# Performance work log

Measured on AMD Instinct MI355X. Metric: run time of the kernel, lower is better.

Reference implementation:

```python
import jax, jax.numpy as jnp
import numpy as np

B, S, L = 256, 512, 128


def setup_inputs() -> dict:
    key = jax.random.key(0)
    k0, k1, k2, k3, k4, k5 = jax.random.split(key, 6)
    features = jax.random.normal(k0, (B, S, L), dtype=jnp.float32)
    attention_mask = jnp.ones((B, S), dtype=jnp.int32)  # all positions valid
    labels = jax.random.randint(k1, (B, S), 0, L)
    confidence = jax.random.uniform(k2, (B,), dtype=jnp.float32)
    start_transitions = jax.random.uniform(k3, (L,), minval=-0.1, maxval=0.1)
    end_transitions = jax.random.uniform(k4, (L,), minval=-0.1, maxval=0.1)
    transitions = jax.random.uniform(k5, (L, L), minval=-0.1, maxval=0.1)
    return {
        "features": features,
        "start_transitions": start_transitions,
        "end_transitions": end_transitions,
        "transitions": transitions,
        "confidence": confidence,
        "attention_mask": attention_mask,
        "labels": labels,
    }


def _crf_loss(features, start_transitions, end_transitions, transitions,
              confidence, attention_mask, labels):
    # time-major, matching torch.swapaxes(features, 0, 1)
    feats = jnp.swapaxes(features, 0, 1)                    # [S,B,L]
    mask = jnp.swapaxes(attention_mask, 0, 1).astype(bool)  # [S,B]
    labs = jnp.swapaxes(jnp.where(labels == -100, 0, labels), 0, 1)  # [S,B]
    bs = feats.shape[1]
    barange = jnp.arange(bs)

    # ---- log numerator (gold path score), fully vectorized over time ----
    emit = jnp.take_along_axis(feats, labs[:, :, None], axis=2)[..., 0]  # [S,B]
    trans_scores = transitions[labs[:-1], labs[1:]]                      # [S-1,B]
    maskf = mask[1:].astype(feats.dtype)
    log_num = (start_transitions[labs[0]] + emit[0]
               + jnp.sum((trans_scores + emit[1:]) * maskf, axis=0))
    seq_lens = mask.sum(axis=0) - 1                                      # [B]
    last_tags = labs[seq_lens, barange]
    log_num = log_num + end_transitions[last_tags]

    # ---- log denominator (partition function) via sequential scan ----
    def step(alpha, xs):
        feat_t, mask_t = xs  # [B,L], [B]
        nxt = jax.nn.logsumexp(
            alpha[:, :, None] + transitions[None, :, :] + feat_t[:, None, :],
            axis=1)
        return jnp.where(mask_t[:, None], nxt, alpha), None

    alpha0 = start_transitions + feats[0]                    # [B,L]
    alpha, _ = jax.lax.scan(step, alpha0, (feats[1:], mask[1:]))
    log_den = jax.nn.logsumexp(alpha + end_transitions, axis=1)  # [B]

    loss = (log_den - log_num) * confidence
    return jnp.mean(loss)


def reference(features, start_transitions, end_transitions, transitions,
              confidence, attention_mask, labels):
    return _crf_loss(features, start_transitions, end_transitions, transitions,
                     confidence, attention_mask, labels)
```

## Files before the change

kernel.cpp:

```cpp
#include <hip/hip_runtime.h>
#include <hip/hip_bf16.h>
#include <math.h>

#define NB 256
#define SS 512
#define LL 128

typedef short bf16x8 __attribute__((ext_vector_type(8)));
typedef float f32x4 __attribute__((ext_vector_type(4)));

template <int P>
__device__ __forceinline__ float swzf(float x) {
    return __int_as_float(__builtin_amdgcn_ds_swizzle(__float_as_int(x), P));
}
__device__ __forceinline__ short f2bf(float f) {
    __hip_bfloat16 h = __float2bfloat16(f);
    short s;
    __builtin_memcpy(&s, &h, 2);
    return s;
}
__device__ __forceinline__ float bf2f(short s) {
    return __int_as_float(((int)(unsigned short)s) << 16);
}

__global__ __launch_bounds__(256, 2) void crf_chain_kernel(
    const float* __restrict__ feats,
    const float* __restrict__ start_t,
    const float* __restrict__ end_t,
    const float* __restrict__ trans,
    const int* __restrict__ mask,
    const int* __restrict__ labels,
    float* __restrict__ ws)
{
    const int bid = blockIdx.x;
    const int b = bid & 255;
    const int isB = bid >> 8;
    const int tid = threadIdx.x;
    const int w = tid >> 6;
    const int L = tid & 63;
    const int l15 = L & 15;
    const int g = L >> 4;
    const int myNt = 2 * w + (g & 1);
    const int p_own = 16 * myNt + l15;

    __shared__ __align__(16) short img[2][LL];
    __shared__ __align__(16) short fS[128 * LL];
    __shared__ int lmask[SS];
    __shared__ float nred[4];
    __shared__ int cred[4];

    float* av = ws;
    float* bv = ws + NB * LL;
    float* eFa = ws + 2 * NB * LL;
    float* eBa = eFa + NB;
    float* lognum = eBa + NB;

    const float* fb = feats + (size_t)b * SS * LL;

    bf16x8 Bf[4][2];
#pragma unroll
    for (int kt = 0; kt < 4; ++kt) {
#pragma unroll
        for (int jj = 0; jj < 2; ++jj) {
            int n = 16 * (2 * w + jj) + l15;
            bf16x8 fr;
#pragma unroll
            for (int j2 = 0; j2 < 8; ++j2) {
                int k = 32 * kt + 8 * g + j2;
                float v = isB ? trans[n * LL + k] : trans[k * LL + n];
                fr[j2] = f2bf(__expf(v));
            }
            Bf[kt][jj] = fr;
        }
    }

    lmask[tid] = mask[b * SS + tid];
    lmask[tid + 256] = mask[b * SS + tid + 256];

    float x;
    if (isB) x = __expf(end_t[p_own]);
    else     x = __expf(start_t[p_own] + fb[p_own]);
    int eacc = 0;

    for (int r = 0; r < 256; ++r) {
        if ((r & 127) == 0) {
            if (r) __syncthreads();
            const int s = r >> 7;
#pragma unroll
            for (int q = 0; q < 16; ++q) {
                int v = tid + 256 * q;
                int slot = v >> 5;
                int pos4 = v & 31;
                int t = isB ? (511 - (128 * s + slot)) : (1 + 128 * s + slot);
                const float4 f4 = *(const float4*)(fb + (size_t)t * LL + 4 * pos4);
                short4 o;
                o.x = f2bf(f4.x); o.y = f2bf(f4.y); o.z = f2bf(f4.z); o.w = f2bf(f4.w);
                *((short4*)&fS[slot * LL + 4 * pos4]) = o;
            }
            __syncthreads();
        }

        const int t = isB ? (511 - r) : (r + 1);
        float ft = bf2f(fS[(r & 127) * LL + p_own]);
        int mt = lmask[t];
        if (r == 255 && !isB) mt = 0;

        float pub = isB ? __expf(ft) * x : x;
        if (g < 2) img[r & 1][p_own] = f2bf(pub);
        __syncthreads();

        const bf16x8* ip = (const bf16x8*)(&img[r & 1][0]);
        bf16x8 a0 = ip[g], a1 = ip[4 + g], a2 = ip[8 + g], a3 = ip[12 + g];
        f32x4 c0 = {0.f, 0.f, 0.f, 0.f}, c1 = {0.f, 0.f, 0.f, 0.f};
        c0 = __builtin_amdgcn_mfma_f32_16x16x32_bf16(a0, Bf[0][0], c0, 0, 0, 0);
        c1 = __builtin_amdgcn_mfma_f32_16x16x32_bf16(a0, Bf[0][1], c1, 0, 0, 0);
        c0 = __builtin_amdgcn_mfma_f32_16x16x32_bf16(a1, Bf[1][0], c0, 0, 0, 0);
        c1 = __builtin_amdgcn_mfma_f32_16x16x32_bf16(a1, Bf[1][1], c1, 0, 0, 0);
        c0 = __builtin_amdgcn_mfma_f32_16x16x32_bf16(a2, Bf[2][0], c0, 0, 0, 0);
        c1 = __builtin_amdgcn_mfma_f32_16x16x32_bf16(a2, Bf[2][1], c1, 0, 0, 0);
        c0 = __builtin_amdgcn_mfma_f32_16x16x32_bf16(a3, Bf[3][0], c0, 0, 0, 0);
        c1 = __builtin_amdgcn_mfma_f32_16x16x32_bf16(a3, Bf[3][1], c1, 0, 0, 0);

        float cpre = (g & 1) ? c1[0] : c0[0];
        float cand = isB ? cpre : __expf(ft) * cpre;
        x = mt ? cand : x;

        if ((r & 7) == 7) {
            float s = 0.f;
#pragma unroll
            for (int i = 0; i < 8; ++i)
                s += bf2f(a0[i]) + bf2f(a1[i]) + bf2f(a2[i]) + bf2f(a3[i]);
            s += swzf<0x401F>(s);
            s += __shfl_xor(s, 32);
            int ex;
            frexpf(s, &ex);
            x = ldexpf(x, -ex);
            eacc += ex;
        }
    }

    if (g < 2) { (isB ? bv : av)[b * LL + p_own] = x; }
    if (tid == 0) { (isB ? eBa : eFa)[b] = (float)eacc; }

    if (isB) {
        const int* lb = labels + b * SS;
        const int* mb = mask + b * SS;
        float term = 0.f;
        int cnt = 0;
#pragma unroll
        for (int rr = 0; rr < 2; ++rr) {
            int tt = tid + rr * 256;
            int l = lb[tt];
            if ((unsigned)l >= LL) l = 0;
            int m = mb[tt];
            cnt += (m != 0);
            if (tt == 0) {
                term += start_t[l] + fb[l];
            } else if (m) {
                int lp = lb[tt - 1];
                if ((unsigned)lp >= LL) lp = 0;
                term += trans[lp * LL + l] + fb[(size_t)tt * LL + l];
            }
        }
#pragma unroll
        for (int o = 1; o < 64; o <<= 1) {
            term += __shfl_xor(term, o);
            cnt += __shfl_xor(cnt, o);
        }
        if (L == 0) { nred[w] = term; cred[w] = cnt; }
        __syncthreads();
        if (tid == 0) {
            float tot = nred[0] + nred[1] + nred[2] + nred[3];
            int c = cred[0] + cred[1] + cred[2] + cred[3];
            int sl = c - 1;
            sl = sl < 0 ? 0 : (sl >= SS ? SS - 1 : sl);
            int lt = lb[sl];
            if ((unsigned)lt >= LL) lt = 0;
            lognum[b] = tot + end_t[lt];
        }
    }
}

__global__ __launch_bounds__(256) void crf_final_kernel(
    const float* __restrict__ ws, const float* __restrict__ conf,
    float* __restrict__ out)
{
    const int tid = threadIdx.x;
    const float* av = ws;
    const float* bv = ws + NB * LL;
    const float* eFa = ws + 2 * NB * LL;
    const float* eBa = eFa + NB;
    const float* ln = eBa + NB;

    const float4* a4 = (const float4*)(av + tid * LL);
    const float4* b4 = (const float4*)(bv + tid * LL);
    float dot = 0.f;
#pragma unroll 8
    for (int k = 0; k < 32; ++k) {
        float4 a = a4[k], bb = b4[k];
        dot += a.x * bb.x + a.y * bb.y + a.z * bb.z + a.w * bb.w;
    }
    float logZ = logf(dot) + 0.69314718055994531f * (eFa[tid] + eBa[tid]);
    float loss = (logZ - ln[tid]) * conf[tid] * (1.0f / NB);

#pragma unroll
    for (int o = 1; o < 64; o <<= 1) loss += __shfl_xor(loss, o);
    __shared__ float red[4];
    if ((tid & 63) == 0) red[tid >> 6] = loss;
    __syncthreads();
    if (tid == 0) out[0] = red[0] + red[1] + red[2] + red[3];
}

extern "C" void kernel_launch(void* const* d_in, const int* in_sizes, int n_in,
                              void* d_out, int out_size, void* d_ws, size_t ws_size,
                              hipStream_t stream) {
    const float* feats  = (const float*)d_in[0];
    const float* startt = (const float*)d_in[1];
    const float* endt   = (const float*)d_in[2];
    const float* trans  = (const float*)d_in[3];
    const float* conf   = (const float*)d_in[4];
    const int*   mask   = (const int*)d_in[5];
    const int*   labels = (const int*)d_in[6];
    float* out = (float*)d_out;
    float* ws = (float*)d_ws;

    hipLaunchKernelGGL(crf_chain_kernel, dim3(2 * NB), dim3(256), 0, stream,
                       feats, startt, endt, trans, mask, labels, ws);
    hipLaunchKernelGGL(crf_final_kernel, dim3(1), dim3(256), 0, stream,
                       ws, conf, out);
}
```

Baseline: 212.1 us.

## Run each CRF chain in a single wavefront with async LDS feature staging

Result: slower. 259.8 us (+22.5%).

```diff
diff --git a/kernel.cpp b/kernel.cpp
--- a/kernel.cpp
+++ b/kernel.cpp
@@ -9,21 +9,24 @@
 typedef short bf16x8 __attribute__((ext_vector_type(8)));
 typedef float f32x4 __attribute__((ext_vector_type(4)));
 
-template <int P>
-__device__ __forceinline__ float swzf(float x) {
-    return __int_as_float(__builtin_amdgcn_ds_swizzle(__float_as_int(x), P));
-}
+typedef __attribute__((address_space(1))) const unsigned int GU32;
+typedef __attribute__((address_space(3))) unsigned int LU32;
+
 __device__ __forceinline__ short f2bf(float f) {
     __hip_bfloat16 h = __float2bfloat16(f);
     short s;
     __builtin_memcpy(&s, &h, 2);
     return s;
 }
-__device__ __forceinline__ float bf2f(short s) {
-    return __int_as_float(((int)(unsigned short)s) << 16);
-}
-
-__global__ __launch_bounds__(256, 2) void crf_chain_kernel(
+
+__device__ __forceinline__ void stage32rows(const float* src, float* dst) {
+#pragma unroll
+    for (int i = 0; i < 16; ++i)
+        __builtin_amdgcn_global_load_lds((GU32*)(src + i * 256),
+                                         (LU32*)(dst + i * 256), 16, 0, 0);
+}
+
+__global__ __launch_bounds__(64, 1) void crf_chain_kernel(
     const float* __restrict__ feats,
     const float* __restrict__ start_t,
     const float* __restrict__ end_t,
@@ -36,123 +39,170 @@
     const int b = bid & 255;
     const int isB = bid >> 8;
     const int tid = threadIdx.x;
-    const int w = tid >> 6;
-    const int L = tid & 63;
-    const int l15 = L & 15;
-    const int g = L >> 4;
-    const int myNt = 2 * w + (g & 1);
-    const int p_own = 16 * myNt + l15;
+    const int l15 = tid & 15;
+    const int g = tid >> 4;
 
     __shared__ __align__(16) short img[2][LL];
-    __shared__ __align__(16) short fS[128 * LL];
+    __shared__ __align__(16) float fS[2][32][LL];
     __shared__ int lmask[SS];
-    __shared__ float nred[4];
-    __shared__ int cred[4];
+
+    const float* fb = feats + (size_t)b * SS * LL;
+
+    {
+        const int rb = isB ? 480 : 1;
+        stage32rows(fb + rb * LL + tid * 4, &fS[0][0][0]);
+    }
+
+#pragma unroll
+    for (int q = 0; q < 8; ++q) lmask[tid + 64 * q] = mask[b * SS + tid + 64 * q];
+
+    bf16x8 Bf[8][4];
+#pragma unroll
+    for (int nt = 0; nt < 8; ++nt) {
+        const int n = 16 * nt + l15;
+#pragma unroll
+        for (int kt = 0; kt < 4; ++kt) {
+            bf16x8 fr;
+#pragma unroll
+            for (int j = 0; j < 8; ++j) {
+                const int k = 32 * kt + 8 * g + j;
+                float tv = isB ? trans[n * LL + k] : trans[k * LL + n];
+                fr[j] = f2bf(__expf(tv));
+            }
+            Bf[nt][kt] = fr;
+        }
+    }
+
+    float v[8];
+#pragma unroll
+    for (int nt = 0; nt < 8; ++nt) {
+        const int p = 16 * nt + l15;
+        v[nt] = isB ? __expf(end_t[p]) : __expf(start_t[p] + fb[p]);
+    }
+
+    asm volatile("s_waitcnt vmcnt(0)" ::: "memory");
+
+    {
+        const int rb = isB ? 448 : 33;
+        stage32rows(fb + rb * LL + tid * 4, &fS[1][0][0]);
+    }
+
+    float eft[8];
+    {
+        const float* fr0 = &fS[0][isB ? 31 : 0][0];
+#pragma unroll
+        for (int nt = 0; nt < 8; ++nt) eft[nt] = __expf(fr0[16 * nt + l15]);
+    }
+
+    int eacc = 0;
+
+    for (int r = 0; r < 256; ++r) {
+        if ((r & 31) == 31 && r != 255)
+            asm volatile("s_waitcnt vmcnt(0)" ::: "memory");
+        if ((r & 31) == 0 && r != 0 && r <= 192) {
+            const int cN = (r >> 5) + 1;
+            const int rb = isB ? (480 - 32 * cN) : (32 * cN + 1);
+            stage32rows(fb + rb * LL + tid * 4, &fS[cN & 1][0][0]);
+        }
+
+        const int t = isB ? (511 - r) : (r + 1);
+        int mt = lmask[t];
+        if (!isB && r == 255) mt = 0;
+
+        float we = (g < 2) ? (g == 0 ? v[0] : v[2]) : (g == 2 ? v[4] : v[6]);
+        float wo = (g < 2) ? (g == 0 ? v[1] : v[3]) : (g == 2 ? v[5] : v[7]);
+        if (isB) {
+            float ee = (g < 2) ? (g == 0 ? eft[0] : eft[2]) : (g == 2 ? eft[4] : eft[6]);
+            float eo = (g < 2) ? (g == 0 ? eft[1] : eft[3]) : (g == 2 ? eft[5] : eft[7]);
+            we *= ee;
+            wo *= eo;
+        }
+        short* ib = &img[r & 1][0];
+        ib[32 * g + l15] = f2bf(we);
+        ib[32 * g + 16 + l15] = f2bf(wo);
+
+        asm volatile("s_waitcnt lgkmcnt(0)" ::: "memory");
+
+        const bf16x8* ip = (const bf16x8*)ib;
+        bf16x8 a0 = ip[g], a1 = ip[4 + g], a2 = ip[8 + g], a3 = ip[12 + g];
+
+        float fnx[8];
+        const int rn = r + 1;
+        if (rn < 256) {
+            const float* frn = &fS[(rn >> 5) & 1][isB ? (31 - (rn & 31)) : (rn & 31)][0];
+#pragma unroll
+            for (int nt = 0; nt < 8; ++nt) fnx[nt] = frn[16 * nt + l15];
+        }
+
+        f32x4 cc[8];
+#pragma unroll
+        for (int nt = 0; nt < 8; ++nt) cc[nt] = (f32x4){0.f, 0.f, 0.f, 0.f};
+#pragma unroll
+        for (int nt = 0; nt < 8; ++nt)
+            cc[nt] = __builtin_amdgcn_mfma_f32_16x16x32_bf16(a0, Bf[nt][0], cc[nt], 0, 0, 0);
+#pragma unroll
+        for (int nt = 0; nt < 8; ++nt)
+            cc[nt] = __builtin_amdgcn_mfma_f32_16x16x32_bf16(a1, Bf[nt][1], cc[nt], 0, 0, 0);
+#pragma unroll
+        for (int nt = 0; nt < 8; ++nt)
+            cc[nt] = __builtin_amdgcn_mfma_f32_16x16x32_bf16(a2, Bf[nt][2], cc[nt], 0, 0, 0);
+#pragma unroll
+        for (int nt = 0; nt < 8; ++nt)
+            cc[nt] = __builtin_amdgcn_mfma_f32_16x16x32_bf16(a3, Bf[nt][3], cc[nt], 0, 0, 0);
+
+#pragma unroll
+        for (int nt = 0; nt < 8; ++nt) {
+            float cpre = cc[nt][0];
+            float cand = isB ? cpre : eft[nt] * cpre;
+            v[nt] = mt ? cand : v[nt];
+        }
+
+        if (rn < 256) {
+#pragma unroll
+            for (int nt = 0; nt < 8; ++nt) eft[nt] = __expf(fnx[nt]);
+        }
+
+        if ((r & 7) == 7) {
+            float s = ((v[0] + v[1]) + (v[2] + v[3])) + ((v[4] + v[5]) + (v[6] + v[7]));
+            s += __shfl_xor(s, 1);
+            s += __shfl_xor(s, 2);
+            s += __shfl_xor(s, 4);
+            s += __shfl_xor(s, 8);
+            int ex;
+            frexpf(s, &ex);
+#pragma unroll
+            for (int nt = 0; nt < 8; ++nt) v[nt] = ldexpf(v[nt], -ex);
+            eacc += ex;
+        }
+    }
 
     float* av = ws;
     float* bv = ws + NB * LL;
     float* eFa = ws + 2 * NB * LL;
     float* eBa = eFa + NB;
-    float* lognum = eBa + NB;
-
-    const float* fb = feats + (size_t)b * SS * LL;
-
-    bf16x8 Bf[4][2];
-#pragma unroll
-    for (int kt = 0; kt < 4; ++kt) {
-#pragma unroll
-        for (int jj = 0; jj < 2; ++jj) {
-            int n = 16 * (2 * w + jj) + l15;
-            bf16x8 fr;
-#pragma unroll
-            for (int j2 = 0; j2 < 8; ++j2) {
-                int k = 32 * kt + 8 * g + j2;
-                float v = isB ? trans[n * LL + k] : trans[k * LL + n];
-                fr[j2] = f2bf(__expf(v));
-            }
-            Bf[kt][jj] = fr;
-        }
-    }
-
-    lmask[tid] = mask[b * SS + tid];
-    lmask[tid + 256] = mask[b * SS + tid + 256];
-
-    float x;
-    if (isB) x = __expf(end_t[p_own]);
-    else     x = __expf(start_t[p_own] + fb[p_own]);
-    int eacc = 0;
-
-    for (int r = 0; r < 256; ++r) {
-        if ((r & 127) == 0) {
-            if (r) __syncthreads();
-            const int s = r >> 7;
-#pragma unroll
-            for (int q = 0; q < 16; ++q) {
-                int v = tid + 256 * q;
-                int slot = v >> 5;
-                int pos4 = v & 31;
-                int t = isB ? (511 - (128 * s + slot)) : (1 + 128 * s + slot);
-                const float4 f4 = *(const float4*)(fb + (size_t)t * LL + 4 * pos4);
-                short4 o;
-                o.x = f2bf(f4.x); o.y = f2bf(f4.y); o.z = f2bf(f4.z); o.w = f2bf(f4.w);
-                *((short4*)&fS[slot * LL + 4 * pos4]) = o;
-            }
-            __syncthreads();
-        }
-
-        const int t = isB ? (511 - r) : (r + 1);
-        float ft = bf2f(fS[(r & 127) * LL + p_own]);
-        int mt = lmask[t];
-        if (r == 255 && !isB) mt = 0;
-
-        float pub = isB ? __expf(ft) * x : x;
-        if (g < 2) img[r & 1][p_own] = f2bf(pub);
-        __syncthreads();
-
-        const bf16x8* ip = (const bf16x8*)(&img[r & 1][0]);
-        bf16x8 a0 = ip[g], a1 = ip[4 + g], a2 = ip[8 + g], a3 = ip[12 + g];
-        f32x4 c0 = {0.f, 0.f, 0.f, 0.f}, c1 = {0.f, 0.f, 0.f, 0.f};
-        c0 = __builtin_amdgcn_mfma_f32_16x16x32_bf16(a0, Bf[0][0], c0, 0, 0, 0);
-        c1 = __builtin_amdgcn_mfma_f32_16x16x32_bf16(a0, Bf[0][1], c1, 0, 0, 0);
-        c0 = __builtin_amdgcn_mfma_f32_16x16x32_bf16(a1, Bf[1][0], c0, 0, 0, 0);
-        c1 = __builtin_amdgcn_mfma_f32_16x16x32_bf16(a1, Bf[1][1], c1, 0, 0, 0);
-        c0 = __builtin_amdgcn_mfma_f32_16x16x32_bf16(a2, Bf[2][0], c0, 0, 0, 0);
-        c1 = __builtin_amdgcn_mfma_f32_16x16x32_bf16(a2, Bf[2][1], c1, 0, 0, 0);
-        c0 = __builtin_amdgcn_mfma_f32_16x16x32_bf16(a3, Bf[3][0], c0, 0, 0, 0);
-        c1 = __builtin_amdgcn_mfma_f32_16x16x32_bf16(a3, Bf[3][1], c1, 0, 0, 0);
-
-        float cpre = (g & 1) ? c1[0] : c0[0];
-        float cand = isB ? cpre : __expf(ft) * cpre;
-        x = mt ? cand : x;
-
-        if ((r & 7) == 7) {
-            float s = 0.f;
-#pragma unroll
-            for (int i = 0; i < 8; ++i)
-                s += bf2f(a0[i]) + bf2f(a1[i]) + bf2f(a2[i]) + bf2f(a3[i]);
-            s += swzf<0x401F>(s);
-            s += __shfl_xor(s, 32);
-            int ex;
-            frexpf(s, &ex);
-            x = ldexpf(x, -ex);
-            eacc += ex;
-        }
-    }
-
-    if (g < 2) { (isB ? bv : av)[b * LL + p_own] = x; }
-    if (tid == 0) { (isB ? eBa : eFa)[b] = (float)eacc; }
-
-    if (isB) {
+    float* nFa = eBa + NB;
+    float* nBa = nFa + NB;
+    float* cFa = nBa + NB;
+    float* cBa = cFa + NB;
+
+    if (g == 0) {
+#pragma unroll
+        for (int nt = 0; nt < 8; ++nt)
+            (isB ? bv : av)[b * LL + 16 * nt + l15] = v[nt];
+    }
+    if (tid == 0) (isB ? eBa : eFa)[b] = (float)eacc;
+
+    {
         const int* lb = labels + b * SS;
         const int* mb = mask + b * SS;
         float term = 0.f;
         int cnt = 0;
 #pragma unroll
-        for (int rr = 0; rr < 2; ++rr) {
-            int tt = tid + rr * 256;
+        for (int q = 0; q < 4; ++q) {
+            const int tt = isB * 256 + tid + 64 * q;
             int l = lb[tt];
             if ((unsigned)l >= LL) l = 0;
-            int m = mb[tt];
+            const int m = mb[tt];
             cnt += (m != 0);
             if (tt == 0) {
                 term += start_t[l] + fb[l];
@@ -167,22 +217,16 @@
             term += __shfl_xor(term, o);
             cnt += __shfl_xor(cnt, o);
         }
-        if (L == 0) { nred[w] = term; cred[w] = cnt; }
-        __syncthreads();
         if (tid == 0) {
-            float tot = nred[0] + nred[1] + nred[2] + nred[3];
-            int c = cred[0] + cred[1] + cred[2] + cred[3];
-            int sl = c - 1;
-            sl = sl < 0 ? 0 : (sl >= SS ? SS - 1 : sl);
-            int lt = lb[sl];
-            if ((unsigned)lt >= LL) lt = 0;
-            lognum[b] = tot + end_t[lt];
+            (isB ? nBa : nFa)[b] = term;
+            (isB ? cBa : cFa)[b] = (float)cnt;
         }
     }
 }
 
 __global__ __launch_bounds__(256) void crf_final_kernel(
     const float* __restrict__ ws, const float* __restrict__ conf,
+    const float* __restrict__ end_t, const int* __restrict__ labels,
     float* __restrict__ out)
 {
     const int tid = threadIdx.x;
@@ -190,7 +234,10 @@
     const float* bv = ws + NB * LL;
     const float* eFa = ws + 2 * NB * LL;
     const float* eBa = eFa + NB;
-    const float* ln = eBa + NB;
+    const float* nFa = eBa + NB;
+    const float* nBa = nFa + NB;
+    const float* cFa = nBa + NB;
+    const float* cBa = cFa + NB;
 
     const float4* a4 = (const float4*)(av + tid * LL);
     const float4* b4 = (const float4*)(bv + tid * LL);
@@ -200,8 +247,14 @@
         float4 a = a4[k], bb = b4[k];
         dot += a.x * bb.x + a.y * bb.y + a.z * bb.z + a.w * bb.w;
     }
+    int c = (int)(cFa[tid] + cBa[tid]);
+    int sl = c - 1;
+    sl = sl < 0 ? 0 : (sl >= SS ? SS - 1 : sl);
+    int lt = labels[tid * SS + sl];
+    if ((unsigned)lt >= LL) lt = 0;
+    float lognum = nFa[tid] + nBa[tid] + end_t[lt];
     float logZ = logf(dot) + 0.69314718055994531f * (eFa[tid] + eBa[tid]);
-    float loss = (logZ - ln[tid]) * conf[tid] * (1.0f / NB);
+    float loss = (logZ - lognum) * conf[tid] * (1.0f / NB);
 
 #pragma unroll
     for (int o = 1; o < 64; o <<= 1) loss += __shfl_xor(loss, o);
@@ -224,8 +277,8 @@
     float* out = (float*)d_out;
     float* ws = (float*)d_ws;
 
-    hipLaunchKernelGGL(crf_chain_kernel, dim3(2 * NB), dim3(256), 0, stream,
+    hipLaunchKernelGGL(crf_chain_kernel, dim3(2 * NB), dim3(64), 0, stream,
                        feats, startt, endt, trans, mask, labels, ws);
     hipLaunchKernelGGL(crf_final_kernel, dim3(1), dim3(256), 0, stream,
-                       ws, conf, out);
-}
+                       ws, conf, endt, labels, out);
+}
```
